# Kernel optimization log

Hardware: AMD Instinct MI355X
Metric: run time of the kernel (lower is better)

## Reference

```python
import jax, jax.numpy as jnp
import numpy as np

B, NQ, NK, DQ, DK, DV, H = 4, 512, 512, 512, 512, 512, 128
NEG_INF = -1e20


def setup_inputs() -> dict:
    key = jax.random.key(0)
    ks = jax.random.split(key, 7)
    Q = jax.random.normal(ks[0], (B, NQ, DQ), dtype=jnp.float32)
    K = jax.random.normal(ks[1], (B, NK, DK), dtype=jnp.float32)
    V = jax.random.normal(ks[2], (B, NK, DV), dtype=jnp.float32)
    # learned params (LazyLinear, bias=False): y = x @ W with W[in, out]
    Wq = jax.random.normal(ks[3], (DQ, H), dtype=jnp.float32) / np.sqrt(DQ)
    Wk = jax.random.normal(ks[4], (DK, H), dtype=jnp.float32) / np.sqrt(DK)
    wv = jax.random.normal(ks[5], (H,), dtype=jnp.float32) / np.sqrt(H)
    valid_lens = jax.random.randint(ks[6], (B,), 1, NK + 1).astype(jnp.int64)
    return {"Q": Q, "K": K, "V": V, "Wq": Wq, "Wk": Wk, "wv": wv,
            "valid_lens": valid_lens}


def reference(Q, K, V, Wq, Wk, wv, valid_lens):
    # Project queries and keys to shared hidden size H
    Qp = Q @ Wq                      # (B, NQ, H)
    Kp = K @ Wk                      # (B, NK, H)
    # Additive (Bahdanau) broadcast: (B, NQ, NK, H)
    S = jnp.tanh(Qp[:, :, None, :] + Kp[:, None, :, :])
    # Linear score to scalar: (B, NQ, NK)
    scores = jnp.einsum('bqkh,h->bqk', S, wv)
    # Mask positions k >= valid_lens[b] (1-D valid_lens broadcast over queries)
    kv_idx = jnp.arange(scores.shape[-1])[None, None, :]
    mask = kv_idx < valid_lens[:, None, None]
    scores = jnp.where(mask, scores, NEG_INF)
    W = jax.nn.softmax(scores, axis=-1)  # dropout rate 0.0 -> identity
    return jnp.einsum('bqk,bkv->bqv', W, V)
```

## Files before the change

kernel.cpp:

```cpp
#include <hip/hip_runtime.h>

#define B_   4
#define NQ_  512
#define NK_  512
#define D_   512
#define H_   128

typedef __attribute__((ext_vector_type(8))) short short8;
typedef __attribute__((ext_vector_type(4))) float f32x4;

__device__ __forceinline__ float fexp2(float x) { return __builtin_amdgcn_exp2f(x); }
__device__ __forceinline__ float frcp(float x)  { return __builtin_amdgcn_rcpf(x); }
__device__ __forceinline__ unsigned short f2bf(float f) {
    unsigned int u = __builtin_bit_cast(unsigned int, f);
    u += 0x7FFFu + ((u >> 16) & 1u);
    return (unsigned short)(u >> 16);
}

#define WS_QKP   0
#define WS_PP    524288
#define WS_WP    4718592
#define WS_WBF   4718848
#define WS_VT    5243136

__global__ __launch_bounds__(256) void proj_kernel(
    const float* __restrict__ Q, const float* __restrict__ K,
    const float* __restrict__ Wq, const float* __restrict__ Wk,
    float* __restrict__ Pp)
{
    const int xb = blockIdx.x;
    const int ks = blockIdx.y;
    const bool isQ = xb < 16;
    const float* __restrict__ X = isQ ? Q : K;
    const float* __restrict__ W = isQ ? Wq : Wk;
    const int r0 = (xb & 15) * 128;
    const int k0 = ks * 64;
    const int t  = threadIdx.x;

    __shared__ float At[32][132];
    __shared__ float Wl[32][132];

    const int cg = t & 15;
    const int rg = t >> 4;
    float acc[8][8] = {};

    for (int kc = 0; kc < 2; ++kc) {
        if (kc) __syncthreads();
        #pragma unroll
        for (int p = 0; p < 4; ++p) {
            const int idx = p * 256 + t;
            const int row = idx & 127;
            const int kq  = (idx >> 7) * 4;
            const float4 v = *reinterpret_cast<const float4*>(
                X + (size_t)(r0 + row) * D_ + k0 + kc * 32 + kq);
            At[kq + 0][row] = v.x; At[kq + 1][row] = v.y;
            At[kq + 2][row] = v.z; At[kq + 3][row] = v.w;
        }
        #pragma unroll
        for (int p = 0; p < 4; ++p) {
            const int idx = p * 256 + t;
            const int kr  = idx >> 5;
            const int c4  = (idx & 31) * 4;
            *reinterpret_cast<float4*>(&Wl[kr][c4]) =
                *reinterpret_cast<const float4*>(
                    W + (size_t)(k0 + kc * 32 + kr) * H_ + c4);
        }
        __syncthreads();

        #pragma unroll 4
        for (int k = 0; k < 32; ++k) {
            const float4 a0 = *reinterpret_cast<const float4*>(&At[k][rg * 8]);
            const float4 a1 = *reinterpret_cast<const float4*>(&At[k][rg * 8 + 4]);
            const float4 b0 = *reinterpret_cast<const float4*>(&Wl[k][cg * 4]);
            const float4 b1 = *reinterpret_cast<const float4*>(&Wl[k][64 + cg * 4]);
            const float aa[8] = {a0.x, a0.y, a0.z, a0.w, a1.x, a1.y, a1.z, a1.w};
            const float bb[8] = {b0.x, b0.y, b0.z, b0.w, b1.x, b1.y, b1.z, b1.w};
            #pragma unroll
            for (int r = 0; r < 8; ++r)
                #pragma unroll
                for (int c = 0; c < 8; ++c)
                    acc[r][c] = fmaf(aa[r], bb[c], acc[r][c]);
        }
    }

    float* __restrict__ dst = Pp + (size_t)ks * (4096 * 128);
    #pragma unroll
    for (int r = 0; r < 8; ++r) {
        const int grow = xb * 128 + rg * 8 + r;
        *reinterpret_cast<float4*>(dst + (size_t)grow * H_ + cg * 4) =
            make_float4(acc[r][0], acc[r][1], acc[r][2], acc[r][3]);
        *reinterpret_cast<float4*>(dst + (size_t)grow * H_ + 64 + cg * 4) =
            make_float4(acc[r][4], acc[r][5], acc[r][6], acc[r][7]);
    }
}

__global__ __launch_bounds__(256) void proj_add_kernel(
    const float* __restrict__ Pp, const float* __restrict__ wv,
    float* __restrict__ QKp, float* __restrict__ wp)
{
    const int i = blockIdx.x * 256 + threadIdx.x;
    const float C2 = 2.88539008177792681472f;
    float4 s = make_float4(0.f, 0.f, 0.f, 0.f);
    #pragma unroll
    for (int p = 0; p < 8; ++p) {
        const float4 v = reinterpret_cast<const float4*>(Pp)[(size_t)p * 131072 + i];
        s.x += v.x; s.y += v.y; s.z += v.z; s.w += v.w;
    }
    s.x *= C2; s.y *= C2; s.z *= C2; s.w *= C2;
    reinterpret_cast<float4*>(QKp)[i] = s;

    if (blockIdx.x == 0 && threadIdx.x < 64) {
        const float2 w2 = reinterpret_cast<const float2*>(wv)[threadIdx.x];
        const float wn0 = -2.0f * w2.x;
        const float wn1 = -2.0f * w2.y;
        reinterpret_cast<float4*>(wp)[threadIdx.x] =
            make_float4(wn0, wn1, wn0 + wn1, 0.0f);
    }
}

__global__ __launch_bounds__(256) void transposeV_kernel(
    const float* __restrict__ V, unsigned short* __restrict__ Vt)
{
    const int kt = blockIdx.x, dt = blockIdx.y, b = blockIdx.z;
    const int t  = threadIdx.x;
    __shared__ float Vl[64][69];

    #pragma unroll
    for (int p = 0; p < 4; ++p) {
        const int idx = p * 256 + t;
        const int r  = idx >> 4;
        const int c4 = (idx & 15) * 4;
        const float4 v = *reinterpret_cast<const float4*>(
            V + ((size_t)b * NK_ + kt * 64 + r) * D_ + dt * 64 + c4);
        Vl[r][c4 + 0] = v.x; Vl[r][c4 + 1] = v.y;
        Vl[r][c4 + 2] = v.z; Vl[r][c4 + 3] = v.w;
    }
    __syncthreads();

    #pragma unroll
    for (int p = 0; p < 4; ++p) {
        const int idx = p * 256 + t;
        const int d  = idx >> 4;
        const int k4 = (idx & 15) * 4;
        ushort4 o;
        o.x = f2bf(Vl[k4 + 0][d]); o.y = f2bf(Vl[k4 + 1][d]);
        o.z = f2bf(Vl[k4 + 2][d]); o.w = f2bf(Vl[k4 + 3][d]);
        *reinterpret_cast<ushort4*>(
            Vt + ((size_t)b * D_ + dt * 64 + d) * NK_ + kt * 64 + k4) = o;
    }
}

__global__ __launch_bounds__(512) void score_softmax_kernel(
    const float* __restrict__ QKp, const float* __restrict__ wp,
    const int* __restrict__ valid_lens, unsigned short* __restrict__ Wbf)
{
    const int b  = blockIdx.y;
    const int q0 = blockIdx.x * 8;
    const int t  = threadIdx.x;
    const int w    = __builtin_amdgcn_readfirstlane(t >> 6);
    const int lane = t & 63;

    __shared__ __align__(16) float4 Ks[64][33];

    const float4* __restrict__ Q4 =
        reinterpret_cast<const float4*>(QKp + (size_t)(b * NQ_ + q0 + w) * H_);
    const float4* __restrict__ wp4 = reinterpret_cast<const float4*>(wp);
    const float4* __restrict__ Kp4 =
        reinterpret_cast<const float4*>(QKp + (size_t)(2048 + b * NK_) * H_);

    float vals[8];

    for (int c = 0; c < 8; ++c) {
        if (c) __syncthreads();
        #pragma unroll
        for (int p = 0; p < 4; ++p) {
            const int idx = p * 512 + t;
            const int r   = idx >> 5;
            const int h4  = idx & 31;
            Ks[r][h4] = Kp4[(size_t)(c * 64 + r) * 32 + h4];
        }
        __syncthreads();

        float s = 0.0f;
        #pragma unroll 8
        for (int g = 0; g < 32; ++g) {
            const float4 kv = Ks[lane][g];
            const float4 qa = Q4[g];
            const float4 wa = wp4[2 * g];
            const float4 wb = wp4[2 * g + 1];
            const float e0 = fexp2(qa.x + kv.x);
            const float e1 = fexp2(qa.y + kv.y);
            const float e2 = fexp2(qa.z + kv.z);
            const float e3 = fexp2(qa.w + kv.w);
            float n0 = fmaf(wa.x, e1, wa.z); n0 = fmaf(wa.y, e0, n0);
            float n1 = fmaf(wb.x, e3, wb.z); n1 = fmaf(wb.y, e2, n1);
            const float d0 = (1.0f + e0) * (1.0f + e1);
            const float d1 = (1.0f + e2) * (1.0f + e3);
            s = fmaf(n0, frcp(d0), s);
            s = fmaf(n1, frcp(d1), s);
        }
        vals[c] = s;
    }

    const int vl = valid_lens[b];
    float m = -1e30f;
    #pragma unroll
    for (int c = 0; c < 8; ++c) {
        const int k = c * 64 + lane;
        vals[c] = (k < vl) ? vals[c] : -1e30f;
        m = fmaxf(m, vals[c]);
    }
    #pragma unroll
    for (int off = 32; off >= 1; off >>= 1)
        m = fmaxf(m, __shfl_xor(m, off, 64));

    const float L2E = 1.44269504088896340736f;
    float e[8];
    float sum = 0.0f;
    #pragma unroll
    for (int c = 0; c < 8; ++c) {
        e[c] = fexp2((vals[c] - m) * L2E);
        sum += e[c];
    }
    #pragma unroll
    for (int off = 32; off >= 1; off >>= 1)
        sum += __shfl_xor(sum, off, 64);

    const float inv = frcp(sum);
    unsigned short* __restrict__ dst = Wbf + (size_t)(b * NQ_ + q0 + w) * NK_;
    #pragma unroll
    for (int c = 0; c < 8; ++c)
        dst[c * 64 + lane] = f2bf(e[c] * inv);
}

__global__ __launch_bounds__(256) void av_gemm_kernel(
    const unsigned short* __restrict__ Wbf, const unsigned short* __restrict__ Vt,
    float* __restrict__ O)
{
    const int c0 = blockIdx.x * 64;
    const int r0 = blockIdx.y * 64;
    const int b  = blockIdx.z;
    const int t  = threadIdx.x;
    const int wave = __builtin_amdgcn_readfirstlane(t >> 6);
    const int lane = t & 63;
    const int m    = lane & 15;
    const int quad = lane >> 4;

    __shared__ unsigned short Al [64][136];
    __shared__ unsigned short Btl[64][136];

    f32x4 acc0 = {0.f,0.f,0.f,0.f}, acc1 = {0.f,0.f,0.f,0.f};
    f32x4 acc2 = {0.f,0.f,0.f,0.f}, acc3 = {0.f,0.f,0.f,0.f};

    for (int kc = 0; kc < 4; ++kc) {
        if (kc) __syncthreads();
        #pragma unroll
        for (int p = 0; p < 4; ++p) {
            const int idx = p * 256 + t;
            const int rl = idx >> 4;
            const int k8 = (idx & 15) * 8;
            *reinterpret_cast<uint4*>(&Al[rl][k8]) =
                *reinterpret_cast<const uint4*>(
                    Wbf + ((size_t)b * NQ_ + r0 + rl) * NK_ + kc * 128 + k8);
            *reinterpret_cast<uint4*>(&Btl[rl][k8]) =
                *reinterpret_cast<const uint4*>(
                    Vt + ((size_t)b * D_ + c0 + rl) * NK_ + kc * 128 + k8);
        }
        __syncthreads();

        #pragma unroll
        for (int sub = 0; sub < 4; ++sub) {
            const int kcol = sub * 32 + quad * 8;
            const short8 a = *reinterpret_cast<const short8*>(&Al[wave * 16 + m][kcol]);
            const short8 b0 = *reinterpret_cast<const short8*>(&Btl[ 0 + m][kcol]);
            const short8 b1 = *reinterpret_cast<const short8*>(&Btl[16 + m][kcol]);
            const short8 b2 = *reinterpret_cast<const short8*>(&Btl[32 + m][kcol]);
            const short8 b3 = *reinterpret_cast<const short8*>(&Btl[48 + m][kcol]);
            acc0 = __builtin_amdgcn_mfma_f32_16x16x32_bf16(a, b0, acc0, 0, 0, 0);
            acc1 = __builtin_amdgcn_mfma_f32_16x16x32_bf16(a, b1, acc1, 0, 0, 0);
            acc2 = __builtin_amdgcn_mfma_f32_16x16x32_bf16(a, b2, acc2, 0, 0, 0);
            acc3 = __builtin_amdgcn_mfma_f32_16x16x32_bf16(a, b3, acc3, 0, 0, 0);
        }
    }

    const size_t rowbase = (size_t)b * NQ_ + r0 + wave * 16 + quad * 4;
    #pragma unroll
    for (int i = 0; i < 4; ++i) {
        float* __restrict__ orow = O + (rowbase + i) * D_ + c0 + m;
        orow[ 0] = acc0[i];
        orow[16] = acc1[i];
        orow[32] = acc2[i];
        orow[48] = acc3[i];
    }
}

extern "C" void kernel_launch(void* const* d_in, const int* in_sizes, int n_in,
                              void* d_out, int out_size, void* d_ws, size_t ws_size,
                              hipStream_t stream) {
    (void)in_sizes; (void)n_in; (void)out_size; (void)ws_size;

    const float* Q   = (const float*)d_in[0];
    const float* K   = (const float*)d_in[1];
    const float* V   = (const float*)d_in[2];
    const float* Wq  = (const float*)d_in[3];
    const float* Wk  = (const float*)d_in[4];
    const float* wv  = (const float*)d_in[5];
    const int*   vl  = (const int*)d_in[6];
    float* out = (float*)d_out;

    float* ws  = (float*)d_ws;
    float* QKp = ws + WS_QKP;
    float* Pp  = ws + WS_PP;
    float* wp  = ws + WS_WP;
    unsigned short* Wbf = (unsigned short*)(ws + WS_WBF);
    unsigned short* Vt  = (unsigned short*)(ws + WS_VT);

    proj_kernel<<<dim3(32, 8), 256, 0, stream>>>(Q, K, Wq, Wk, Pp);
    proj_add_kernel<<<dim3(512), 256, 0, stream>>>(Pp, wv, QKp, wp);
    transposeV_kernel<<<dim3(8, 8, 4), 256, 0, stream>>>(V, Vt);
    score_softmax_kernel<<<dim3(64, 4), 512, 0, stream>>>(QKp, wp, vl, Wbf);
    av_gemm_kernel<<<dim3(8, 8, 4), 256, 0, stream>>>(Wbf, Vt, out);
}
```

Before: 131.4 us.

## Split score kernel across key chunks and fuse softmax into AV GEMM

Merges the V transpose into the projection kernel so both run in one launch. The score kernel now splits the keys into four 128-wide chunks per block, giving four times as many blocks, and writes raw fp32 scores. The tanh math is rearranged so each group of four hidden units needs only one reciprocal. Softmax max and sum are recomputed per row inside the AV GEMM, which builds bf16 probabilities on the fly with 512 threads. The cost is an fp32 score round trip through global memory and repeated softmax work in each of the eight column blocks.

```diff
diff --git a/kernel.cpp b/kernel.cpp
--- a/kernel.cpp
+++ b/kernel.cpp
@@ -20,77 +20,110 @@
 #define WS_QKP   0
 #define WS_PP    524288
 #define WS_WP    4718592
-#define WS_WBF   4718848
-#define WS_VT    5243136
-
-__global__ __launch_bounds__(256) void proj_kernel(
+#define WS_SC    4718848
+#define WS_VT    5767424
+
+__global__ __launch_bounds__(256) void prep_kernel(
     const float* __restrict__ Q, const float* __restrict__ K,
     const float* __restrict__ Wq, const float* __restrict__ Wk,
-    float* __restrict__ Pp)
+    const float* __restrict__ V,
+    float* __restrict__ Pp, unsigned short* __restrict__ Vt)
 {
-    const int xb = blockIdx.x;
-    const int ks = blockIdx.y;
-    const bool isQ = xb < 16;
-    const float* __restrict__ X = isQ ? Q : K;
-    const float* __restrict__ W = isQ ? Wq : Wk;
-    const int r0 = (xb & 15) * 128;
-    const int k0 = ks * 64;
-    const int t  = threadIdx.x;
-
-    __shared__ float At[32][132];
-    __shared__ float Wl[32][132];
-
-    const int cg = t & 15;
-    const int rg = t >> 4;
-    float acc[8][8] = {};
-
-    for (int kc = 0; kc < 2; ++kc) {
-        if (kc) __syncthreads();
+    __shared__ float smem[2 * 32 * 132];
+    const int t = threadIdx.x;
+
+    if (blockIdx.x < 32) {
+        const int xb = blockIdx.x;
+        const int ks = blockIdx.y;
+        const bool isQ = xb < 16;
+        const float* __restrict__ X = isQ ? Q : K;
+        const float* __restrict__ W = isQ ? Wq : Wk;
+        const int r0 = (xb & 15) * 128;
+        const int k0 = ks * 64;
+
+        float (*At)[132] = (float(*)[132])smem;
+        float (*Wl)[132] = (float(*)[132])(smem + 32*132);
+
+        const int cg = t & 15;
+        const int rg = t >> 4;
+        float acc[8][8] = {};
+
+        for (int kc = 0; kc < 2; ++kc) {
+            if (kc) __syncthreads();
+            #pragma unroll
+            for (int p = 0; p < 4; ++p) {
+                const int idx = p * 256 + t;
+                const int row = idx & 127;
+                const int kq  = (idx >> 7) * 4;
+                const float4 v = *reinterpret_cast<const float4*>(
+                    X + (size_t)(r0 + row) * D_ + k0 + kc * 32 + kq);
+                At[kq + 0][row] = v.x; At[kq + 1][row] = v.y;
+                At[kq + 2][row] = v.z; At[kq + 3][row] = v.w;
+            }
+            #pragma unroll
+            for (int p = 0; p < 4; ++p) {
+                const int idx = p * 256 + t;
+                const int kr  = idx >> 5;
+                const int c4  = (idx & 31) * 4;
+                *reinterpret_cast<float4*>(&Wl[kr][c4]) =
+                    *reinterpret_cast<const float4*>(
+                        W + (size_t)(k0 + kc * 32 + kr) * H_ + c4);
+            }
+            __syncthreads();
+
+            #pragma unroll 4
+            for (int k = 0; k < 32; ++k) {
+                const float4 a0 = *reinterpret_cast<const float4*>(&At[k][rg * 8]);
+                const float4 a1 = *reinterpret_cast<const float4*>(&At[k][rg * 8 + 4]);
+                const float4 b0 = *reinterpret_cast<const float4*>(&Wl[k][cg * 4]);
+                const float4 b1 = *reinterpret_cast<const float4*>(&Wl[k][64 + cg * 4]);
+                const float aa[8] = {a0.x, a0.y, a0.z, a0.w, a1.x, a1.y, a1.z, a1.w};
+                const float bb[8] = {b0.x, b0.y, b0.z, b0.w, b1.x, b1.y, b1.z, b1.w};
+                #pragma unroll
+                for (int r = 0; r < 8; ++r)
+                    #pragma unroll
+                    for (int c = 0; c < 8; ++c)
+                        acc[r][c] = fmaf(aa[r], bb[c], acc[r][c]);
+            }
+        }
+
+        float* __restrict__ dst = Pp + (size_t)blockIdx.y * (4096 * 128);
+        #pragma unroll
+        for (int r = 0; r < 8; ++r) {
+            const int grow = xb * 128 + rg * 8 + r;
+            *reinterpret_cast<float4*>(dst + (size_t)grow * H_ + cg * 4) =
+                make_float4(acc[r][0], acc[r][1], acc[r][2], acc[r][3]);
+            *reinterpret_cast<float4*>(dst + (size_t)grow * H_ + 64 + cg * 4) =
+                make_float4(acc[r][4], acc[r][5], acc[r][6], acc[r][7]);
+        }
+    } else {
+        const int id = (blockIdx.x - 32) * 8 + blockIdx.y;
+        const int kt = id & 7, dt = (id >> 3) & 7, b = id >> 6;
+        float (*Vl)[69] = (float(*)[69])smem;
+
         #pragma unroll
         for (int p = 0; p < 4; ++p) {
             const int idx = p * 256 + t;
-            const int row = idx & 127;
-            const int kq  = (idx >> 7) * 4;
+            const int r  = idx >> 4;
+            const int c4 = (idx & 15) * 4;
             const float4 v = *reinterpret_cast<const float4*>(
-                X + (size_t)(r0 + row) * D_ + k0 + kc * 32 + kq);
-            At[kq + 0][row] = v.x; At[kq + 1][row] = v.y;
-            At[kq + 2][row] = v.z; At[kq + 3][row] = v.w;
-        }
+                V + ((size_t)b * NK_ + kt * 64 + r) * D_ + dt * 64 + c4);
+            Vl[r][c4 + 0] = v.x; Vl[r][c4 + 1] = v.y;
+            Vl[r][c4 + 2] = v.z; Vl[r][c4 + 3] = v.w;
+        }
+        __syncthreads();
+
         #pragma unroll
         for (int p = 0; p < 4; ++p) {
             const int idx = p * 256 + t;
-            const int kr  = idx >> 5;
-            const int c4  = (idx & 31) * 4;
-            *reinterpret_cast<float4*>(&Wl[kr][c4]) =
-                *reinterpret_cast<const float4*>(
-                    W + (size_t)(k0 + kc * 32 + kr) * H_ + c4);
-        }
-        __syncthreads();
-
-        #pragma unroll 4
-        for (int k = 0; k < 32; ++k) {
-            const float4 a0 = *reinterpret_cast<const float4*>(&At[k][rg * 8]);
-            const float4 a1 = *reinterpret_cast<const float4*>(&At[k][rg * 8 + 4]);
-            const float4 b0 = *reinterpret_cast<const float4*>(&Wl[k][cg * 4]);
-            const float4 b1 = *reinterpret_cast<const float4*>(&Wl[k][64 + cg * 4]);
-            const float aa[8] = {a0.x, a0.y, a0.z, a0.w, a1.x, a1.y, a1.z, a1.w};
-            const float bb[8] = {b0.x, b0.y, b0.z, b0.w, b1.x, b1.y, b1.z, b1.w};
-            #pragma unroll
-            for (int r = 0; r < 8; ++r)
-                #pragma unroll
-                for (int c = 0; c < 8; ++c)
-                    acc[r][c] = fmaf(aa[r], bb[c], acc[r][c]);
-        }
-    }
-
-    float* __restrict__ dst = Pp + (size_t)ks * (4096 * 128);
-    #pragma unroll
-    for (int r = 0; r < 8; ++r) {
-        const int grow = xb * 128 + rg * 8 + r;
-        *reinterpret_cast<float4*>(dst + (size_t)grow * H_ + cg * 4) =
-            make_float4(acc[r][0], acc[r][1], acc[r][2], acc[r][3]);
-        *reinterpret_cast<float4*>(dst + (size_t)grow * H_ + 64 + cg * 4) =
-            make_float4(acc[r][4], acc[r][5], acc[r][6], acc[r][7]);
+            const int d  = idx >> 4;
+            const int k4 = (idx & 15) * 4;
+            ushort4 o;
+            o.x = f2bf(Vl[k4 + 0][d]); o.y = f2bf(Vl[k4 + 1][d]);
+            o.z = f2bf(Vl[k4 + 2][d]); o.w = f2bf(Vl[k4 + 3][d]);
+            *reinterpret_cast<ushort4*>(
+                Vt + ((size_t)b * D_ + dt * 64 + d) * NK_ + kt * 64 + k4) = o;
+        }
     }
 }
 
@@ -118,71 +151,38 @@
     }
 }
 
-__global__ __launch_bounds__(256) void transposeV_kernel(
-    const float* __restrict__ V, unsigned short* __restrict__ Vt)
+__global__ __launch_bounds__(512, 8) void score_kernel(
+    const float* __restrict__ QKp, const float* __restrict__ wp,
+    float* __restrict__ Sc)
 {
-    const int kt = blockIdx.x, dt = blockIdx.y, b = blockIdx.z;
-    const int t  = threadIdx.x;
-    __shared__ float Vl[64][69];
-
-    #pragma unroll
-    for (int p = 0; p < 4; ++p) {
-        const int idx = p * 256 + t;
-        const int r  = idx >> 4;
-        const int c4 = (idx & 15) * 4;
-        const float4 v = *reinterpret_cast<const float4*>(
-            V + ((size_t)b * NK_ + kt * 64 + r) * D_ + dt * 64 + c4);
-        Vl[r][c4 + 0] = v.x; Vl[r][c4 + 1] = v.y;
-        Vl[r][c4 + 2] = v.z; Vl[r][c4 + 3] = v.w;
-    }
-    __syncthreads();
-
-    #pragma unroll
-    for (int p = 0; p < 4; ++p) {
-        const int idx = p * 256 + t;
-        const int d  = idx >> 4;
-        const int k4 = (idx & 15) * 4;
-        ushort4 o;
-        o.x = f2bf(Vl[k4 + 0][d]); o.y = f2bf(Vl[k4 + 1][d]);
-        o.z = f2bf(Vl[k4 + 2][d]); o.w = f2bf(Vl[k4 + 3][d]);
-        *reinterpret_cast<ushort4*>(
-            Vt + ((size_t)b * D_ + dt * 64 + d) * NK_ + kt * 64 + k4) = o;
-    }
-}
-
-__global__ __launch_bounds__(512) void score_softmax_kernel(
-    const float* __restrict__ QKp, const float* __restrict__ wp,
-    const int* __restrict__ valid_lens, unsigned short* __restrict__ Wbf)
-{
-    const int b  = blockIdx.y;
-    const int q0 = blockIdx.x * 8;
-    const int t  = threadIdx.x;
+    const int b    = blockIdx.x >> 6;
+    const int ks   = blockIdx.y;
+    const int t    = threadIdx.x;
     const int w    = __builtin_amdgcn_readfirstlane(t >> 6);
     const int lane = t & 63;
+    const int row  = blockIdx.x * 8 + w;
 
     __shared__ __align__(16) float4 Ks[64][33];
 
     const float4* __restrict__ Q4 =
-        reinterpret_cast<const float4*>(QKp + (size_t)(b * NQ_ + q0 + w) * H_);
+        reinterpret_cast<const float4*>(QKp + (size_t)row * H_);
     const float4* __restrict__ wp4 = reinterpret_cast<const float4*>(wp);
     const float4* __restrict__ Kp4 =
         reinterpret_cast<const float4*>(QKp + (size_t)(2048 + b * NK_) * H_);
 
-    float vals[8];
-
-    for (int c = 0; c < 8; ++c) {
+    for (int c = 0; c < 2; ++c) {
         if (c) __syncthreads();
         #pragma unroll
         for (int p = 0; p < 4; ++p) {
             const int idx = p * 512 + t;
             const int r   = idx >> 5;
             const int h4  = idx & 31;
-            Ks[r][h4] = Kp4[(size_t)(c * 64 + r) * 32 + h4];
+            Ks[r][h4] = Kp4[(size_t)(ks * 128 + c * 64 + r) * 32 + h4];
         }
         __syncthreads();
 
         float s = 0.0f;
-        #pragma unroll 8
+        #pragma unroll 4
         for (int g = 0; g < 32; ++g) {
             const float4 kv = Ks[lane][g];
             const float4 qa = Q4[g];
@@ -192,50 +192,22 @@
             const float e1 = fexp2(qa.y + kv.y);
             const float e2 = fexp2(qa.z + kv.z);
             const float e3 = fexp2(qa.w + kv.w);
-            float n0 = fmaf(wa.x, e1, wa.z); n0 = fmaf(wa.y, e0, n0);
-            float n1 = fmaf(wb.x, e3, wb.z); n1 = fmaf(wb.y, e2, n1);
-            const float d0 = (1.0f + e0) * (1.0f + e1);
-            const float d1 = (1.0f + e2) * (1.0f + e3);
-            s = fmaf(n0, frcp(d0), s);
-            s = fmaf(n1, frcp(d1), s);
-        }
-        vals[c] = s;
-    }
-
-    const int vl = valid_lens[b];
-    float m = -1e30f;
-    #pragma unroll
-    for (int c = 0; c < 8; ++c) {
-        const int k = c * 64 + lane;
-        vals[c] = (k < vl) ? vals[c] : -1e30f;
-        m = fmaxf(m, vals[c]);
-    }
-    #pragma unroll
-    for (int off = 32; off >= 1; off >>= 1)
-        m = fmaxf(m, __shfl_xor(m, off, 64));
-
-    const float L2E = 1.44269504088896340736f;
-    float e[8];
-    float sum = 0.0f;
-    #pragma unroll
-    for (int c = 0; c < 8; ++c) {
-        e[c] = fexp2((vals[c] - m) * L2E);
-        sum += e[c];
-    }
-    #pragma unroll
-    for (int off = 32; off >= 1; off >>= 1)
-        sum += __shfl_xor(sum, off, 64);
-
-    const float inv = frcp(sum);
-    unsigned short* __restrict__ dst = Wbf + (size_t)(b * NQ_ + q0 + w) * NK_;
-    #pragma unroll
-    for (int c = 0; c < 8; ++c)
-        dst[c * 64 + lane] = f2bf(e[c] * inv);
-}
-
-__global__ __launch_bounds__(256) void av_gemm_kernel(
-    const unsigned short* __restrict__ Wbf, const unsigned short* __restrict__ Vt,
-    float* __restrict__ O)
+            const float p01 = fmaf(e0, e1, e0 + e1);
+            const float p23 = fmaf(e2, e3, e2 + e3);
+            const float D01 = 1.0f + p01;
+            const float D23 = 1.0f + p23;
+            const float n01 = fmaf(wa.y, e0, fmaf(wa.x, e1, wa.z));
+            const float n23 = fmaf(wb.y, e2, fmaf(wb.x, e3, wb.z));
+            const float N   = fmaf(n23, D01, n01 * D23);
+            s = fmaf(N, frcp(D01 * D23), s);
+        }
+        Sc[(size_t)row * NK_ + ks * 128 + c * 64 + lane] = s;
+    }
+}
+
+__global__ __launch_bounds__(512) void gemm_softmax_kernel(
+    const float* __restrict__ Sc, const unsigned short* __restrict__ Vt,
+    const int* __restrict__ valid_lens, float* __restrict__ O)
 {
     const int c0 = blockIdx.x * 64;
     const int r0 = blockIdx.y * 64;
@@ -245,52 +217,93 @@
     const int lane = t & 63;
     const int m    = lane & 15;
     const int quad = lane >> 4;
+    const int vl   = valid_lens[b];
+    const float L2E = 1.44269504088896340736f;
 
     __shared__ unsigned short Al [64][136];
     __shared__ unsigned short Btl[64][136];
+    __shared__ float rowM[64], rowI[64];
+
+    #pragma unroll
+    for (int rr = 0; rr < 8; ++rr) {
+        const int rl = wave * 8 + rr;
+        const float4* __restrict__ srow =
+            reinterpret_cast<const float4*>(Sc + ((size_t)b * NQ_ + r0 + rl) * NK_);
+        const float4 v0 = srow[lane * 2];
+        const float4 v1 = srow[lane * 2 + 1];
+        float v[8] = {v0.x, v0.y, v0.z, v0.w, v1.x, v1.y, v1.z, v1.w};
+        float mx = -1e30f;
+        #pragma unroll
+        for (int j = 0; j < 8; ++j) {
+            v[j] = (lane * 8 + j < vl) ? v[j] : -1e30f;
+            mx = fmaxf(mx, v[j]);
+        }
+        #pragma unroll
+        for (int off = 32; off >= 1; off >>= 1)
+            mx = fmaxf(mx, __shfl_xor(mx, off, 64));
+        float sum = 0.0f;
+        #pragma unroll
+        for (int j = 0; j < 8; ++j)
+            sum += fexp2((v[j] - mx) * L2E);
+        #pragma unroll
+        for (int off = 32; off >= 1; off >>= 1)
+            sum += __shfl_xor(sum, off, 64);
+        if (lane == 0) { rowM[rl] = mx; rowI[rl] = frcp(sum); }
+    }
 
     f32x4 acc0 = {0.f,0.f,0.f,0.f}, acc1 = {0.f,0.f,0.f,0.f};
-    f32x4 acc2 = {0.f,0.f,0.f,0.f}, acc3 = {0.f,0.f,0.f,0.f};
 
     for (int kc = 0; kc < 4; ++kc) {
-        if (kc) __syncthreads();
-        #pragma unroll
-        for (int p = 0; p < 4; ++p) {
-            const int idx = p * 256 + t;
+        __syncthreads();
+        #pragma unroll
+        for (int p = 0; p < 2; ++p) {
+            const int idx = p * 512 + t;
             const int rl = idx >> 4;
             const int k8 = (idx & 15) * 8;
-            *reinterpret_cast<uint4*>(&Al[rl][k8]) =
-                *reinterpret_cast<const uint4*>(
-                    Wbf + ((size_t)b * NQ_ + r0 + rl) * NK_ + kc * 128 + k8);
             *reinterpret_cast<uint4*>(&Btl[rl][k8]) =
                 *reinterpret_cast<const uint4*>(
                     Vt + ((size_t)b * D_ + c0 + rl) * NK_ + kc * 128 + k8);
         }
+        #pragma unroll
+        for (int p = 0; p < 4; ++p) {
+            const int idx = p * 512 + t;
+            const int rl = idx >> 5;
+            const int kg = idx & 31;
+            const float4 s4 = reinterpret_cast<const float4*>(
+                Sc + ((size_t)b * NQ_ + r0 + rl) * NK_)[kc * 32 + kg];
+            const float mr = rowM[rl];
+            const float ir = rowI[rl];
+            const int kk = kc * 128 + kg * 4;
+            ushort4 o;
+            o.x = (kk + 0 < vl) ? f2bf(fexp2((s4.x - mr) * L2E) * ir) : (unsigned short)0;
+            o.y = (kk + 1 < vl) ? f2bf(fexp2((s4.y - mr) * L2E) * ir) : (unsigned short)0;
+            o.z = (kk + 2 < vl) ? f2bf(fexp2((s4.z - mr) * L2E) * ir) : (unsigned short)0;
+            o.w = (kk + 3 < vl) ? f2bf(fexp2((s4.w - mr) * L2E) * ir) : (unsigned short)0;
+            *reinterpret_cast<ushort4*>(&Al[rl][kg * 4]) = o;
+        }
         __syncthreads();
 
         #pragma unroll
-        for (int sub = 0; sub < 4; ++sub) {
-            const int kcol = sub * 32 + quad * 8;
-            const short8 a = *reinterpret_cast<const short8*>(&Al[wave * 16 + m][kcol]);
-            const short8 b0 = *reinterpret_cast<const short8*>(&Btl[ 0 + m][kcol]);
-            const short8 b1 = *reinterpret_cast<const short8*>(&Btl[16 + m][kcol]);
-            const short8 b2 = *reinterpret_cast<const short8*>(&Btl[32 + m][kcol]);
-            const short8 b3 = *reinterpret_cast<const short8*>(&Btl[48 + m][kcol]);
+        for (int s = 0; s < 4; ++s) {
+            const int kcol = s * 32 + quad * 8;
+            const short8 a  = *reinterpret_cast<const short8*>(
+                &Al[(wave & 3) * 16 + m][kcol]);
+            const short8 b0 = *reinterpret_cast<const short8*>(
+                &Btl[(wave >> 2) * 32 + m][kcol]);
+            const short8 b1 = *reinterpret_cast<const short8*>(
+                &Btl[(wave >> 2) * 32 + 16 + m][kcol]);
             acc0 = __builtin_amdgcn_mfma_f32_16x16x32_bf16(a, b0, acc0, 0, 0, 0);
             acc1 = __builtin_amdgcn_mfma_f32_16x16x32_bf16(a, b1, acc1, 0, 0, 0);
-            acc2 = __builtin_amdgcn_mfma_f32_16x16x32_bf16(a, b2, acc2, 0, 0, 0);
-            acc3 = __builtin_amdgcn_mfma_f32_16x16x32_bf16(a, b3, acc3, 0, 0, 0);
-        }
-    }
-
-    const size_t rowbase = (size_t)b * NQ_ + r0 + wave * 16 + quad * 4;
+        }
+    }
+
+    const size_t rowbase = (size_t)b * NQ_ + r0 + (wave & 3) * 16 + quad * 4;
+    const int colbase = c0 + (wave >> 2) * 32 + m;
     #pragma unroll
     for (int i = 0; i < 4; ++i) {
-        float* __restrict__ orow = O + (rowbase + i) * D_ + c0 + m;
+        float* __restrict__ orow = O + (rowbase + i) * D_ + colbase;
         orow[ 0] = acc0[i];
         orow[16] = acc1[i];
-        orow[32] = acc2[i];
-        orow[48] = acc3[i];
     }
 }
 
@@ -312,12 +325,11 @@
     float* QKp = ws + WS_QKP;
     float* Pp  = ws + WS_PP;
     float* wp  = ws + WS_WP;
-    unsigned short* Wbf = (unsigned short*)(ws + WS_WBF);
-    unsigned short* Vt  = (unsigned short*)(ws + WS_VT);
-
-    proj_kernel<<<dim3(32, 8), 256, 0, stream>>>(Q, K, Wq, Wk, Pp);
+    float* Sc  = ws + WS_SC;
+    unsigned short* Vt = (unsigned short*)(ws + WS_VT);
+
+    prep_kernel<<<dim3(64, 8), 256, 0, stream>>>(Q, K, Wq, Wk, V, Pp, Vt);
     proj_add_kernel<<<dim3(512), 256, 0, stream>>>(Pp, wv, QKp, wp);
-    transposeV_kernel<<<dim3(8, 8, 4), 256, 0, stream>>>(V, Vt);
-    score_softmax_kernel<<<dim3(64, 4), 512, 0, stream>>>(QKp, wp, vl, Wbf);
-    av_gemm_kernel<<<dim3(8, 8, 4), 256, 0, stream>>>(Wbf, Vt, out);
-}
+    score_kernel<<<dim3(256, 4), 512, 0, stream>>>(QKp, wp, Sc);
+    gemm_softmax_kernel<<<dim3(8, 8, 4), 512, 0, stream>>>(Sc, Vt, vl, out);
+}
```

Result: slower. 135.2 us (+2.9%).

## Split score and softmax, tile keys across blocks, fuse V transpose into projection

Applied to the files above, without the earlier changes.

The projection GEMM and the V transpose/bf16 conversion are merged into one launch, with blocks branching on blockIdx. The fused score+softmax kernel is split in two. The score kernel now tiles keys into 128-wide slices across a second grid dimension, giving 512 blocks instead of 256. Each wave computes two query rows per loaded K tile and combines two tanh pairs under one reciprocal, cutting rcp count and reusing K loads. A separate softmax kernel reads fp32 scores back from workspace, which adds a round-trip of about 4 MB, in exchange for more parallelism and fewer transcendental ops.

```diff
diff --git a/kernel.cpp b/kernel.cpp
--- a/kernel.cpp
+++ b/kernel.cpp
@@ -17,80 +17,115 @@
     return (unsigned short)(u >> 16);
 }
 
+
 #define WS_QKP   0
 #define WS_PP    524288
 #define WS_WP    4718592
-#define WS_WBF   4718848
-#define WS_VT    5243136
-
-__global__ __launch_bounds__(256) void proj_kernel(
+#define WS_SC    4718848
+#define WS_VT    5767424
+#define WS_WBF   6291712
+
+__global__ __launch_bounds__(256) void prep_kernel(
     const float* __restrict__ Q, const float* __restrict__ K,
     const float* __restrict__ Wq, const float* __restrict__ Wk,
-    float* __restrict__ Pp)
-{
-    const int xb = blockIdx.x;
-    const int ks = blockIdx.y;
-    const bool isQ = xb < 16;
-    const float* __restrict__ X = isQ ? Q : K;
-    const float* __restrict__ W = isQ ? Wq : Wk;
-    const int r0 = (xb & 15) * 128;
-    const int k0 = ks * 64;
-    const int t  = threadIdx.x;
-
-    __shared__ float At[32][132];
-    __shared__ float Wl[32][132];
-
-    const int cg = t & 15;
-    const int rg = t >> 4;
-    float acc[8][8] = {};
-
-    for (int kc = 0; kc < 2; ++kc) {
-        if (kc) __syncthreads();
+    const float* __restrict__ V,
+    float* __restrict__ Pp, unsigned short* __restrict__ Vt)
+{
+    __shared__ float smem[2 * 32 * 132];
+    const int t = threadIdx.x;
+
+    if (blockIdx.x < 32) {
+        const int xb = blockIdx.x;
+        const int ks = blockIdx.y;
+        const bool isQ = xb < 16;
+        const float* __restrict__ X = isQ ? Q : K;
+        const float* __restrict__ W = isQ ? Wq : Wk;
+        const int r0 = (xb & 15) * 128;
+        const int k0 = ks * 64;
+
+        float (*At)[132] = (float(*)[132])smem;
+        float (*Wl)[132] = (float(*)[132])(smem + 32 * 132);
+
+        const int cg = t & 15;
+        const int rg = t >> 4;
+        float acc[8][8] = {};
+
+        for (int kc = 0; kc < 2; ++kc) {
+            if (kc) __syncthreads();
+            #pragma unroll
+            for (int p = 0; p < 4; ++p) {
+                const int idx = p * 256 + t;
+                const int row = idx & 127;
+                const int kq  = (idx >> 7) * 4;
+                const float4 v = *reinterpret_cast<const float4*>(
+                    X + (size_t)(r0 + row) * D_ + k0 + kc * 32 + kq);
+                At[kq + 0][row] = v.x; At[kq + 1][row] = v.y;
+                At[kq + 2][row] = v.z; At[kq + 3][row] = v.w;
+            }
+            #pragma unroll
+            for (int p = 0; p < 4; ++p) {
+                const int idx = p * 256 + t;
+                const int kr  = idx >> 5;
+                const int c4  = (idx & 31) * 4;
+                *reinterpret_cast<float4*>(&Wl[kr][c4]) =
+                    *reinterpret_cast<const float4*>(
+                        W + (size_t)(k0 + kc * 32 + kr) * H_ + c4);
+            }
+            __syncthreads();
+
+            #pragma unroll 4
+            for (int k = 0; k < 32; ++k) {
+                const float4 a0 = *reinterpret_cast<const float4*>(&At[k][rg * 8]);
+                const float4 a1 = *reinterpret_cast<const float4*>(&At[k][rg * 8 + 4]);
+                const float4 b0 = *reinterpret_cast<const float4*>(&Wl[k][cg * 4]);
+                const float4 b1 = *reinterpret_cast<const float4*>(&Wl[k][64 + cg * 4]);
+                const float aa[8] = {a0.x, a0.y, a0.z, a0.w, a1.x, a1.y, a1.z, a1.w};
+                const float bb[8] = {b0.x, b0.y, b0.z, b0.w, b1.x, b1.y, b1.z, b1.w};
+                #pragma unroll
+                for (int r = 0; r < 8; ++r)
+                    #pragma unroll
+                    for (int c = 0; c < 8; ++c)
+                        acc[r][c] = fmaf(aa[r], bb[c], acc[r][c]);
+            }
+        }
+
+        float* __restrict__ dst = Pp + (size_t)blockIdx.y * (4096 * 128);
+        #pragma unroll
+        for (int r = 0; r < 8; ++r) {
+            const int grow = xb * 128 + rg * 8 + r;
+            *reinterpret_cast<float4*>(dst + (size_t)grow * H_ + cg * 4) =
+                make_float4(acc[r][0], acc[r][1], acc[r][2], acc[r][3]);
+            *reinterpret_cast<float4*>(dst + (size_t)grow * H_ + 64 + cg * 4) =
+                make_float4(acc[r][4], acc[r][5], acc[r][6], acc[r][7]);
+        }
+    } else {
+        const int id = (blockIdx.x - 32) * 8 + blockIdx.y;
+        const int kt = id & 7, dt = (id >> 3) & 7, b = id >> 6;
+        float (*Vl)[69] = (float(*)[69])smem;
+
         #pragma unroll
         for (int p = 0; p < 4; ++p) {
             const int idx = p * 256 + t;
-            const int row = idx & 127;
-            const int kq  = (idx >> 7) * 4;
+            const int r  = idx >> 4;
+            const int c4 = (idx & 15) * 4;
             const float4 v = *reinterpret_cast<const float4*>(
-                X + (size_t)(r0 + row) * D_ + k0 + kc * 32 + kq);
-            At[kq + 0][row] = v.x; At[kq + 1][row] = v.y;
-            At[kq + 2][row] = v.z; At[kq + 3][row] = v.w;
-        }
+                V + ((size_t)b * NK_ + kt * 64 + r) * D_ + dt * 64 + c4);
+            Vl[r][c4 + 0] = v.x; Vl[r][c4 + 1] = v.y;
+            Vl[r][c4 + 2] = v.z; Vl[r][c4 + 3] = v.w;
+        }
+        __syncthreads();
+
         #pragma unroll
         for (int p = 0; p < 4; ++p) {
             const int idx = p * 256 + t;
-            const int kr  = idx >> 5;
-            const int c4  = (idx & 31) * 4;
-            *reinterpret_cast<float4*>(&Wl[kr][c4]) =
-                *reinterpret_cast<const float4*>(
-                    W + (size_t)(k0 + kc * 32 + kr) * H_ + c4);
-        }
-        __syncthreads();
-
-        #pragma unroll 4
-        for (int k = 0; k < 32; ++k) {
-            const float4 a0 = *reinterpret_cast<const float4*>(&At[k][rg * 8]);
-            const float4 a1 = *reinterpret_cast<const float4*>(&At[k][rg * 8 + 4]);
-            const float4 b0 = *reinterpret_cast<const float4*>(&Wl[k][cg * 4]);
-            const float4 b1 = *reinterpret_cast<const float4*>(&Wl[k][64 + cg * 4]);
-            const float aa[8] = {a0.x, a0.y, a0.z, a0.w, a1.x, a1.y, a1.z, a1.w};
-            const float bb[8] = {b0.x, b0.y, b0.z, b0.w, b1.x, b1.y, b1.z, b1.w};
-            #pragma unroll
-            for (int r = 0; r < 8; ++r)
-                #pragma unroll
-                for (int c = 0; c < 8; ++c)
-                    acc[r][c] = fmaf(aa[r], bb[c], acc[r][c]);
-        }
-    }
-
-    float* __restrict__ dst = Pp + (size_t)ks * (4096 * 128);
-    #pragma unroll
-    for (int r = 0; r < 8; ++r) {
-        const int grow = xb * 128 + rg * 8 + r;
-        *reinterpret_cast<float4*>(dst + (size_t)grow * H_ + cg * 4) =
-            make_float4(acc[r][0], acc[r][1], acc[r][2], acc[r][3]);
-        *reinterpret_cast<float4*>(dst + (size_t)grow * H_ + 64 + cg * 4) =
-            make_float4(acc[r][4], acc[r][5], acc[r][6], acc[r][7]);
+            const int d  = idx >> 4;
+            const int k4 = (idx & 15) * 4;
+            ushort4 o;
+            o.x = f2bf(Vl[k4 + 0][d]); o.y = f2bf(Vl[k4 + 1][d]);
+            o.z = f2bf(Vl[k4 + 2][d]); o.w = f2bf(Vl[k4 + 3][d]);
+            *reinterpret_cast<ushort4*>(
+                Vt + ((size_t)b * D_ + dt * 64 + d) * NK_ + kt * 64 + k4) = o;
+        }
     }
 }
 
@@ -118,119 +153,124 @@
     }
 }
 
-__global__ __launch_bounds__(256) void transposeV_kernel(
-    const float* __restrict__ V, unsigned short* __restrict__ Vt)
-{
-    const int kt = blockIdx.x, dt = blockIdx.y, b = blockIdx.z;
-    const int t  = threadIdx.x;
-    __shared__ float Vl[64][69];
-
-    #pragma unroll
-    for (int p = 0; p < 4; ++p) {
-        const int idx = p * 256 + t;
-        const int r  = idx >> 4;
-        const int c4 = (idx & 15) * 4;
-        const float4 v = *reinterpret_cast<const float4*>(
-            V + ((size_t)b * NK_ + kt * 64 + r) * D_ + dt * 64 + c4);
-        Vl[r][c4 + 0] = v.x; Vl[r][c4 + 1] = v.y;
-        Vl[r][c4 + 2] = v.z; Vl[r][c4 + 3] = v.w;
-    }
-    __syncthreads();
-
-    #pragma unroll
-    for (int p = 0; p < 4; ++p) {
-        const int idx = p * 256 + t;
-        const int d  = idx >> 4;
-        const int k4 = (idx & 15) * 4;
-        ushort4 o;
-        o.x = f2bf(Vl[k4 + 0][d]); o.y = f2bf(Vl[k4 + 1][d]);
-        o.z = f2bf(Vl[k4 + 2][d]); o.w = f2bf(Vl[k4 + 3][d]);
-        *reinterpret_cast<ushort4*>(
-            Vt + ((size_t)b * D_ + dt * 64 + d) * NK_ + kt * 64 + k4) = o;
-    }
-}
-
-__global__ __launch_bounds__(512) void score_softmax_kernel(
+__global__ __launch_bounds__(512, 4) void score_kernel(
     const float* __restrict__ QKp, const float* __restrict__ wp,
-    const int* __restrict__ valid_lens, unsigned short* __restrict__ Wbf)
-{
-    const int b  = blockIdx.y;
-    const int q0 = blockIdx.x * 8;
-    const int t  = threadIdx.x;
+    float* __restrict__ Sc)
+{
+    const int rb   = blockIdx.x;
+    const int ks   = blockIdx.y;
+    const int b    = rb >> 5;
+    const int t    = threadIdx.x;
     const int w    = __builtin_amdgcn_readfirstlane(t >> 6);
     const int lane = t & 63;
+    const int row0 = rb * 16 + w * 2;
 
     __shared__ __align__(16) float4 Ks[64][33];
 
-    const float4* __restrict__ Q4 =
-        reinterpret_cast<const float4*>(QKp + (size_t)(b * NQ_ + q0 + w) * H_);
+    const float4* __restrict__ Q4a =
+        reinterpret_cast<const float4*>(QKp + (size_t)row0 * H_);
+    const float4* __restrict__ Q4b = Q4a + 32;
     const float4* __restrict__ wp4 = reinterpret_cast<const float4*>(wp);
     const float4* __restrict__ Kp4 =
         reinterpret_cast<const float4*>(QKp + (size_t)(2048 + b * NK_) * H_);
 
-    float vals[8];
-
-    for (int c = 0; c < 8; ++c) {
+    for (int c = 0; c < 2; ++c) {
         if (c) __syncthreads();
         #pragma unroll
         for (int p = 0; p < 4; ++p) {
             const int idx = p * 512 + t;
             const int r   = idx >> 5;
             const int h4  = idx & 31;
-            Ks[r][h4] = Kp4[(size_t)(c * 64 + r) * 32 + h4];
+            Ks[r][h4] = Kp4[(size_t)(ks * 128 + c * 64 + r) * 32 + h4];
         }
         __syncthreads();
 
-        float s = 0.0f;
-        #pragma unroll 8
+        float sA = 0.0f, sB = 0.0f;
+        #pragma unroll 4
         for (int g = 0; g < 32; ++g) {
             const float4 kv = Ks[lane][g];
-            const float4 qa = Q4[g];
+            const float4 qa = Q4a[g];
+            const float4 qb = Q4b[g];
             const float4 wa = wp4[2 * g];
             const float4 wb = wp4[2 * g + 1];
-            const float e0 = fexp2(qa.x + kv.x);
-            const float e1 = fexp2(qa.y + kv.y);
-            const float e2 = fexp2(qa.z + kv.z);
-            const float e3 = fexp2(qa.w + kv.w);
-            float n0 = fmaf(wa.x, e1, wa.z); n0 = fmaf(wa.y, e0, n0);
-            float n1 = fmaf(wb.x, e3, wb.z); n1 = fmaf(wb.y, e2, n1);
-            const float d0 = (1.0f + e0) * (1.0f + e1);
-            const float d1 = (1.0f + e2) * (1.0f + e3);
-            s = fmaf(n0, frcp(d0), s);
-            s = fmaf(n1, frcp(d1), s);
-        }
-        vals[c] = s;
-    }
-
-    const int vl = valid_lens[b];
+            {
+                const float e0 = fexp2(qa.x + kv.x);
+                const float e1 = fexp2(qa.y + kv.y);
+                const float e2 = fexp2(qa.z + kv.z);
+                const float e3 = fexp2(qa.w + kv.w);
+                const float D01 = 1.0f + fmaf(e0, e1, e0 + e1);
+                const float D23 = 1.0f + fmaf(e2, e3, e2 + e3);
+                const float n01 = fmaf(wa.y, e0, fmaf(wa.x, e1, wa.z));
+                const float n23 = fmaf(wb.y, e2, fmaf(wb.x, e3, wb.z));
+                const float N   = fmaf(n23, D01, n01 * D23);
+                sA = fmaf(N, frcp(D01 * D23), sA);
+            }
+            {
+                const float e0 = fexp2(qb.x + kv.x);
+                const float e1 = fexp2(qb.y + kv.y);
+                const float e2 = fexp2(qb.z + kv.z);
+                const float e3 = fexp2(qb.w + kv.w);
+                const float D01 = 1.0f + fmaf(e0, e1, e0 + e1);
+                const float D23 = 1.0f + fmaf(e2, e3, e2 + e3);
+                const float n01 = fmaf(wa.y, e0, fmaf(wa.x, e1, wa.z));
+                const float n23 = fmaf(wb.y, e2, fmaf(wb.x, e3, wb.z));
+                const float N   = fmaf(n23, D01, n01 * D23);
+                sB = fmaf(N, frcp(D01 * D23), sB);
+            }
+        }
+        const size_t so = (size_t)row0 * NK_ + ks * 128 + c * 64 + lane;
+        Sc[so]       = sA;
+        Sc[so + NK_] = sB;
+    }
+}
+
+__global__ __launch_bounds__(256) void softmax_kernel(
+    const float* __restrict__ Sc, const int* __restrict__ valid_lens,
+    unsigned short* __restrict__ Wbf)
+{
+    const int row  = blockIdx.x * 4 + (threadIdx.x >> 6);
+    const int lane = threadIdx.x & 63;
+    const int b    = row >> 9;
+    const int vl   = valid_lens[b];
+    const float L2E = 1.44269504088896340736f;
+
+    const float4* __restrict__ srow =
+        reinterpret_cast<const float4*>(Sc + (size_t)row * NK_);
+    const float4 v0 = srow[lane * 2];
+    const float4 v1 = srow[lane * 2 + 1];
+    float v[8] = {v0.x, v0.y, v0.z, v0.w, v1.x, v1.y, v1.z, v1.w};
+
+    const int k0 = lane * 8;
     float m = -1e30f;
     #pragma unroll
-    for (int c = 0; c < 8; ++c) {
-        const int k = c * 64 + lane;
-        vals[c] = (k < vl) ? vals[c] : -1e30f;
-        m = fmaxf(m, vals[c]);
+    for (int j = 0; j < 8; ++j) {
+        v[j] = (k0 + j < vl) ? v[j] : -1e30f;
+        m = fmaxf(m, v[j]);
     }
     #pragma unroll
     for (int off = 32; off >= 1; off >>= 1)
         m = fmaxf(m, __shfl_xor(m, off, 64));
 
-    const float L2E = 1.44269504088896340736f;
     float e[8];
     float sum = 0.0f;
     #pragma unroll
-    for (int c = 0; c < 8; ++c) {
-        e[c] = fexp2((vals[c] - m) * L2E);
-        sum += e[c];
+    for (int j = 0; j < 8; ++j) {
+        e[j] = fexp2((v[j] - m) * L2E);
+        sum += e[j];
     }
     #pragma unroll
     for (int off = 32; off >= 1; off >>= 1)
         sum += __shfl_xor(sum, off, 64);
 
     const float inv = frcp(sum);
-    unsigned short* __restrict__ dst = Wbf + (size_t)(b * NQ_ + q0 + w) * NK_;
-    #pragma unroll
-    for (int c = 0; c < 8; ++c)
-        dst[c * 64 + lane] = f2bf(e[c] * inv);
+    unsigned short* __restrict__ dst = Wbf + (size_t)row * NK_ + k0;
+    ushort4 o0, o1;
+    o0.x = f2bf(e[0] * inv); o0.y = f2bf(e[1] * inv);
+    o0.z = f2bf(e[2] * inv); o0.w = f2bf(e[3] * inv);
+    o1.x = f2bf(e[4] * inv); o1.y = f2bf(e[5] * inv);
+    o1.z = f2bf(e[6] * inv); o1.w = f2bf(e[7] * inv);
+    *reinterpret_cast<ushort4*>(dst)     = o0;
+    *reinterpret_cast<ushort4*>(dst + 4) = o1;
 }
 
 __global__ __launch_bounds__(256) void av_gemm_kernel(
@@ -312,12 +352,13 @@
     float* QKp = ws + WS_QKP;
     float* Pp  = ws + WS_PP;
     float* wp  = ws + WS_WP;
+    float* Sc  = ws + WS_SC;
+    unsigned short* Vt  = (unsigned short*)(ws + WS_VT);
     unsigned short* Wbf = (unsigned short*)(ws + WS_WBF);
-    unsigned short* Vt  = (unsigned short*)(ws + WS_VT);
-
-    proj_kernel<<<dim3(32, 8), 256, 0, stream>>>(Q, K, Wq, Wk, Pp);
+
+    prep_kernel<<<dim3(64, 8), 256, 0, stream>>>(Q, K, Wq, Wk, V, Pp, Vt);
     proj_add_kernel<<<dim3(512), 256, 0, stream>>>(Pp, wv, QKp, wp);
-    transposeV_kernel<<<dim3(8, 8, 4), 256, 0, stream>>>(V, Vt);
-    score_softmax_kernel<<<dim3(64, 4), 512, 0, stream>>>(QKp, wp, vl, Wbf);
+    score_kernel<<<dim3(128, 4), 512, 0, stream>>>(QKp, wp, Sc);
+    softmax_kernel<<<dim3(512), 256, 0, stream>>>(Sc, vl, Wbf);
     av_gemm_kernel<<<dim3(8, 8, 4), 256, 0, stream>>>(Wbf, Vt, out);
 }
```

After: 125.7 us. 4.4% less time.
